# Performance work log

Measured on AMD Instinct MI355X. Metric: run time of the kernel, lower is better.

## Reference

```python
import jax, jax.numpy as jnp
import numpy as np

MASK_FILL = -1e9  # masked_fill_value (avoids NaNs vs -inf)

def setup_inputs() -> dict:
    key = jax.random.key(0)
    k1, k2, k3 = jax.random.split(key, 3)
    B, L, H, E = 4, 2048, 16, 128
    S, D = L, E
    queries = jax.random.normal(k1, (B, L, H, E), dtype=jnp.float32)
    keys = jax.random.normal(k2, (B, S, H, E), dtype=jnp.float32)
    values = jax.random.normal(k3, (B, S, H, D), dtype=jnp.float32)
    return {"queries": queries, "keys": keys, "values": values}

def reference(queries, keys, values):
    B, L, H, E = queries.shape
    S = keys.shape[1]
    scale = 1.0 / jnp.sqrt(jnp.asarray(E, queries.dtype))
    # compute_scores: dot-product scores (B,H,L,S)
    scores = jnp.einsum('blhe,bshe->bhls', queries, keys)
    # causal mask (mask_flag=True, attn_mask=None -> TriangularCausalMask)
    causal = jnp.triu(jnp.ones((L, S), dtype=bool), k=1)  # True above diagonal = masked
    scores = jnp.where(causal[None, None, :, :], MASK_FILL, scores)
    # scale * scores -> softmax (dropout p=0, eval)
    A = jax.nn.softmax(scale * scores, axis=-1)
    # combine_values: (B,H,L,S) x (B,S,H,D) -> (B,L,H,D)
    V = jnp.einsum('bhls,bshd->blhd', A, values)
    return V
```

## Files before the change

### kernel.cpp

```cpp
#include <hip/hip_runtime.h>
#include <hip/hip_bf16.h>

typedef __attribute__((ext_vector_type(4))) float f32x4;
typedef __attribute__((ext_vector_type(2))) float f32x2v;
typedef __attribute__((ext_vector_type(16))) float f32x16;
typedef __attribute__((ext_vector_type(8))) short s16x8;
typedef __attribute__((ext_vector_type(4))) short s16x4;
typedef __attribute__((ext_vector_type(4))) unsigned u32x4v;
typedef __attribute__((ext_vector_type(2))) int i32x2;

static constexpr int Bb = 4, Ll = 2048, Hh = 16, Ee = 128;
static constexpr int RS = Hh * Ee;
static constexpr float SCALE = 0.088388347648318447f;
static constexpr float LOG2E = 1.4426950408889634f;
static constexpr float SCL = SCALE * LOG2E;
static constexpr float MOFF = 26.0f;

static constexpr int KROW = 272;
static constexpr int KBYTES = 32 * KROW;
static constexpr int VROW = 80;
static constexpr int VBYTES = 128 * VROW;
static constexpr int BUFSZ = KBYTES + VBYTES;

__device__ __forceinline__ unsigned pk2bf(float lo, float hi) {
  float2 t = make_float2(lo, hi);
  __hip_bfloat162 b2 = __float22bfloat162_rn(t);
  union { __hip_bfloat162 b; unsigned u; } cv; cv.b = b2;
  return cv.u;
}

__device__ __forceinline__ s16x8 pack8(float a0, float a1, float a2, float a3,
                                       float a4, float a5, float a6, float a7) {
  u32x4v u = { pk2bf(a0,a1), pk2bf(a2,a3), pk2bf(a4,a5), pk2bf(a6,a7) };
  return *(s16x8*)&u;
}

__device__ __forceinline__ void plswap(int &x, int &y, int h5) {
#if __has_builtin(__builtin_amdgcn_permlane32_swap)
  i32x2 r = __builtin_amdgcn_permlane32_swap(x, y, false, false);
  x = r[0]; y = r[1];
#else
  int px = __shfl_xor(x, 32, 64);
  int py = __shfl_xor(y, 32, 64);
  int nx = h5 ? py : x;
  int ny = h5 ? y : px;
  x = nx; y = ny;
#endif
}

__device__ __forceinline__ s16x8 mkpa(float p0, float p1, float p2, float p3,
                                      float p4, float p5, float p6, float p7, int h5) {
  int uA = (int)pk2bf(p0, p1), uB = (int)pk2bf(p2, p3);
  int uC = (int)pk2bf(p4, p5), uD = (int)pk2bf(p6, p7);
  plswap(uA, uC, h5);
  plswap(uB, uD, h5);
  u32x4v u = { (unsigned)uA, (unsigned)uB, (unsigned)uC, (unsigned)uD };
  return *(s16x8*)&u;
}

__device__ __forceinline__ void gl_lds16(const short* g, short* l) {
  __builtin_amdgcn_global_load_lds((const __attribute__((address_space(1))) void*)g,
                                   (__attribute__((address_space(3))) void*)l, 16, 0, 0);
}

__global__ __launch_bounds__(256) void conv_k(const float* __restrict__ src, short* __restrict__ dst) {
  size_t i = ((size_t)blockIdx.x * 256 + threadIdx.x) * 8;
  f32x4 a = *(const f32x4*)(src + i);
  f32x4 b = *(const f32x4*)(src + i + 4);
  *(s16x8*)(dst + i) = pack8(a[0],a[1],a[2],a[3],b[0],b[1],b[2],b[3]);
}

__global__ __launch_bounds__(256) void conv_vt(const float* __restrict__ V, unsigned* __restrict__ Vt32) {
  const int bh = blockIdx.x >> 4, s0 = (blockIdx.x & 15) * 128;
  const int b = bh >> 4, h = bh & 15;
  const int w = threadIdx.x >> 6, lane = threadIdx.x & 63;
  const float* base = V + ((size_t)(b * Ll + s0 + 32 * w)) * RS + h * Ee + 2 * lane;
  unsigned w0[16], w1[16];
#pragma unroll
  for (int j = 0; j < 16; ++j) {
    f32x2v a = *(const f32x2v*)(base + (size_t)(2 * j) * RS);
    f32x2v c = *(const f32x2v*)(base + (size_t)(2 * j + 1) * RS);
    w0[j] = pk2bf(a[0], c[0]);
    w1[j] = pk2bf(a[1], c[1]);
  }
  unsigned* r0 = Vt32 + ((size_t)(bh * 128 + 2 * lane)) * 1024 + (s0 + 32 * w) / 2;
  unsigned* r1 = r0 + 1024;
#pragma unroll
  for (int jj = 0; jj < 4; ++jj) {
    *(u32x4v*)(r0 + 4 * jj) = (u32x4v){w0[4*jj], w0[4*jj+1], w0[4*jj+2], w0[4*jj+3]};
    *(u32x4v*)(r1 + 4 * jj) = (u32x4v){w1[4*jj], w1[4*jj+1], w1[4*jj+2], w1[4*jj+3]};
  }
}

__global__ __launch_bounds__(256, 3)
void attn_main(const float* __restrict__ Qg, const short* __restrict__ Kws,
               const short* __restrict__ Vtws, float* __restrict__ Og) {
  const int phys = blockIdx.x;
  const int qi = ((phys >> 6) & 1) ? (phys >> 7) : (15 - (phys >> 7));
  const int bh = phys & 63;
  const int b = bh >> 4, h = bh & 15;
  const int qb = qi * 128;
  const int tid = threadIdx.x, w = tid >> 6, l = tid & 63;
  const int l31 = l & 31, h5 = l >> 5;

  __shared__ __align__(16) short smem[BUFSZ];

  s16x8 qfrag[8];
  {
    const float* qp = Qg + ((size_t)(b * Ll + qb + 32 * w + l31)) * RS + h * Ee;
#pragma unroll
    for (int ks = 0; ks < 8; ++ks) {
      const int e0 = 16 * ks + 8 * h5;
      f32x4 f0 = *(const f32x4*)(qp + e0);
      f32x4 f1 = *(const f32x4*)(qp + e0 + 4);
      qfrag[ks] = pack8(f0[0]*SCL, f0[1]*SCL, f0[2]*SCL, f0[3]*SCL,
                        f1[0]*SCL, f1[1]*SCL, f1[2]*SCL, f1[3]*SCL);
    }
  }

  f32x16 acc[4];
#pragma unroll
  for (int dt = 0; dt < 4; ++dt)
#pragma unroll
    for (int r = 0; r < 16; ++r) acc[dt][r] = 0.f;
  float lacc = 0.f;

  const short* skp[3]; const short* svp[3];
  int kdst[3], vdst[3];
#pragma unroll
  for (int j = 0; j < 3; ++j) {
    const int kid = (j < 2) ? (w * 136 + 64 * j + l) : (w * 136 + 128 + (l & 7));
    const int kr = kid / 17;
    int ksl = kid % 17; if (ksl == 16) ksl = 0;
    skp[j] = Kws + ((size_t)(b * Ll + kr)) * 2048 + h * 128 + ksl * 8;
    kdst[j] = kid * 16;
    const int vid = (j < 2) ? (w * 160 + 64 * j + l) : (w * 160 + 128 + (l & 31));
    const int vr = vid / 5;
    int vsl = vid % 5; if (vsl == 4) vsl = 0;
    svp[j] = Vtws + ((size_t)(bh * 128 + vr)) * 2048 + vsl * 8;
    vdst[j] = KBYTES + vid * 16;
  }

#define STAGE(cb, kvb) do { \
    gl_lds16(skp[0] + (size_t)(kvb) * 2048, (short*)((char*)smem + (cb) + kdst[0])); \
    gl_lds16(skp[1] + (size_t)(kvb) * 2048, (short*)((char*)smem + (cb) + kdst[1])); \
    if (l < 8)  gl_lds16(skp[2] + (size_t)(kvb) * 2048, (short*)((char*)smem + (cb) + kdst[2])); \
    gl_lds16(svp[0] + (kvb), (short*)((char*)smem + (cb) + vdst[0])); \
    gl_lds16(svp[1] + (kvb), (short*)((char*)smem + (cb) + vdst[1])); \
    if (l < 32) gl_lds16(svp[2] + (kvb), (short*)((char*)smem + (cb) + vdst[2])); \
  } while (0)

  const int ntiles = 4 * qi + 4;
  const int tmaxw = 4 * qi + w;

  STAGE(0, 0);

  for (int t = 0; t < ntiles; ++t) {
    const int cbase = (t & 1) ? BUFSZ : 0;
    if (t + 1 < ntiles) {
      STAGE(cbase ? 0 : BUFSZ, 32 * (t + 1));
      asm volatile("s_waitcnt vmcnt(6)" ::: "memory");
    } else {
      asm volatile("s_waitcnt vmcnt(0)" ::: "memory");
    }
    __builtin_amdgcn_s_barrier();
    __builtin_amdgcn_sched_barrier(0);

    if (t <= tmaxw) {
      f32x16 s;
#pragma unroll
      for (int r = 0; r < 16; ++r) s[r] = 0.f;
      __builtin_amdgcn_s_setprio(1);
#pragma unroll
      for (int ks = 0; ks < 8; ++ks) {
        s16x8 a = *(const s16x8*)((const char*)smem + cbase + l31 * KROW + h5 * 16 + ks * 32);
        s = __builtin_amdgcn_mfma_f32_32x32x16_bf16(a, qfrag[ks], s, 0, 0, 0);
      }
      __builtin_amdgcn_s_setprio(0);

      if (t == tmaxw) {
#pragma unroll
        for (int r = 0; r < 16; ++r) {
          const int kvl = (r & 3) + 8 * (r >> 2) + 4 * h5;
          if (kvl > l31) s[r] = -3.0e38f;
        }
      }

      float pv[16];
#pragma unroll
      for (int r = 0; r < 16; ++r) { const float p2 = exp2f(s[r] - MOFF); pv[r] = p2; lacc += p2; }
      s16x8 pa0 = mkpa(pv[0], pv[1], pv[2], pv[3], pv[4], pv[5], pv[6], pv[7], h5);
      s16x8 pa1 = mkpa(pv[8], pv[9], pv[10], pv[11], pv[12], pv[13], pv[14], pv[15], h5);

      __builtin_amdgcn_s_setprio(1);
#pragma unroll
      for (int dt = 0; dt < 4; ++dt) {
        const int vb = cbase + KBYTES + dt * (32 * VROW) + l31 * VROW + h5 * 16;
        s16x8 av0 = *(const s16x8*)((const char*)smem + vb);
        acc[dt] = __builtin_amdgcn_mfma_f32_32x32x16_bf16(av0, pa0, acc[dt], 0, 0, 0);
        s16x8 av1 = *(const s16x8*)((const char*)smem + vb + 32);
        acc[dt] = __builtin_amdgcn_mfma_f32_32x32x16_bf16(av1, pa1, acc[dt], 0, 0, 0);
      }
      __builtin_amdgcn_s_setprio(0);
    }
    __builtin_amdgcn_sched_barrier(0);
    __builtin_amdgcn_s_barrier();
  }
#undef STAGE

  float lsum;
  {
    int pb = __builtin_bit_cast(int, lacc), pc = pb;
    plswap(pb, pc, h5);
    lsum = __builtin_bit_cast(float, pb) + __builtin_bit_cast(float, pc);
  }
  const float linv = 1.0f / lsum;

  float* orow = Og + ((size_t)(b * Ll + qb + 32 * w + l31)) * RS + h * Ee;
#pragma unroll
  for (int dt = 0; dt < 4; ++dt)
#pragma unroll
    for (int g = 0; g < 4; ++g) {
      f32x4 v = { acc[dt][4*g] * linv, acc[dt][4*g+1] * linv,
                  acc[dt][4*g+2] * linv, acc[dt][4*g+3] * linv };
      *(f32x4*)(orow + dt * 32 + g * 8 + h5 * 4) = v;
    }
}

static constexpr int VPAD = 66;
__device__ __forceinline__ short f2bf(float f) {
  union { float f; unsigned u; } x; x.f = f;
  unsigned r = x.u + 0x7FFFu + ((x.u >> 16) & 1u);
  return (short)(r >> 16);
}
__global__ __launch_bounds__(256, 4)
void attn_fwd(const float* __restrict__ Qg, const float* __restrict__ Kg,
              const float* __restrict__ Vg, float* __restrict__ Og) {
  const int qi = blockIdx.x;
  const int bh = blockIdx.y;
  const int b = bh >> 4, h = bh & 15;
  const int qb = qi * 64;
  const int tid = threadIdx.x, wave = tid >> 6, lane = tid & 63, lo = lane & 15, hi = lane >> 4;
  __shared__ __align__(16) short Klds[64 * 128];
  __shared__ __align__(16) short Vt[128 * VPAD];
  const float* Qb_ = Qg + (size_t)b * Ll * RS + h * Ee;
  const float* Kb_ = Kg + (size_t)b * Ll * RS + h * Ee;
  const float* Vb_ = Vg + (size_t)b * Ll * RS + h * Ee;
  float* Ob_ = Og + (size_t)b * Ll * RS + h * Ee;
  s16x8 qfrag[4];
  {
    const float* qp = Qb_ + (size_t)(qb + wave * 16 + lo) * RS;
#pragma unroll
    for (int ks = 0; ks < 4; ++ks) {
      const int e0 = 32 * ks + 8 * hi;
      f32x4 f0 = *(const f32x4*)(qp + e0);
      f32x4 f1 = *(const f32x4*)(qp + e0 + 4);
      qfrag[ks] = pack8(f0[0]*SCALE, f0[1]*SCALE, f0[2]*SCALE, f0[3]*SCALE,
                        f1[0]*SCALE, f1[1]*SCALE, f1[2]*SCALE, f1[3]*SCALE);
    }
  }
  f32x4 acc[8];
#pragma unroll
  for (int nt = 0; nt < 8; ++nt) acc[nt] = (f32x4){0.f, 0.f, 0.f, 0.f};
  float mrun = -3.0e38f, lrun = 0.f;
  const int r0 = tid >> 4, c0 = (tid & 15) * 8;
  for (int kvb = 0; kvb <= qb; kvb += 64) {
    __syncthreads();
#pragma unroll
    for (int rr4 = 0; rr4 < 4; ++rr4) {
      const int rr = r0 + 16 * rr4;
      const float* kp = Kb_ + (size_t)(kvb + rr) * RS + c0;
      f32x4 f0 = *(const f32x4*)kp;
      f32x4 f1 = *(const f32x4*)(kp + 4);
      const int off = (rr * 256 + c0 * 2) ^ ((rr & 7) << 4);
      *(s16x8*)((char*)Klds + off) = pack8(f0[0],f0[1],f0[2],f0[3],f1[0],f1[1],f1[2],f1[3]);
    }
#pragma unroll
    for (int kk = 0; kk < 2; ++kk) {
      const int kv0 = (r0 * 2 + kk) * 2;
      const float* vp0 = Vb_ + (size_t)(kvb + kv0) * RS + c0;
      const float* vp1 = vp0 + RS;
      f32x4 a0 = *(const f32x4*)vp0, a1 = *(const f32x4*)(vp0 + 4);
      f32x4 b0 = *(const f32x4*)vp1, b1 = *(const f32x4*)(vp1 + 4);
#pragma unroll
      for (int jj = 0; jj < 4; ++jj)
        *(unsigned*)&Vt[(c0 + jj) * VPAD + kv0] = pk2bf(a0[jj], b0[jj]);
#pragma unroll
      for (int jj = 0; jj < 4; ++jj)
        *(unsigned*)&Vt[(c0 + 4 + jj) * VPAD + kv0] = pk2bf(a1[jj], b1[jj]);
    }
    __syncthreads();
    const bool diag = (kvb == qb);
    f32x4 st[4];
#pragma unroll
    for (int mt = 0; mt < 4; ++mt) {
      f32x4 a4 = (f32x4){0.f, 0.f, 0.f, 0.f};
#pragma unroll
      for (int ks = 0; ks < 4; ++ks) {
        const int row = 16 * mt + lo;
        const int off = (row * 256 + (32 * ks + 8 * hi) * 2) ^ ((row & 7) << 4);
        s16x8 a = *(const s16x8*)((const char*)Klds + off);
        a4 = __builtin_amdgcn_mfma_f32_16x16x32_bf16(a, qfrag[ks], a4, 0, 0, 0);
      }
      st[mt] = a4;
    }
    if (diag) {
      const int qg = 16 * wave + lo;
#pragma unroll
      for (int mt = 0; mt < 4; ++mt)
#pragma unroll
        for (int r = 0; r < 4; ++r)
          if (16 * mt + 4 * hi + r > qg) st[mt][r] = -3.0e38f;
    }
    float mx = -3.0e38f;
#pragma unroll
    for (int mt = 0; mt < 4; ++mt)
#pragma unroll
      for (int r = 0; r < 4; ++r) mx = fmaxf(mx, st[mt][r]);
    mx = fmaxf(mx, __shfl_xor(mx, 16, 64));
    mx = fmaxf(mx, __shfl_xor(mx, 32, 64));
    const float mnew = fmaxf(mrun, mx);
    const float alpha = exp2f((mrun - mnew) * LOG2E);
    float psum = 0.f;
    s16x4 pf[4];
#pragma unroll
    for (int mt = 0; mt < 4; ++mt)
#pragma unroll
      for (int r = 0; r < 4; ++r) {
        const float p = exp2f((st[mt][r] - mnew) * LOG2E);
        psum += p;
        pf[mt][r] = f2bf(p);
      }
    psum += __shfl_xor(psum, 16, 64);
    psum += __shfl_xor(psum, 32, 64);
    lrun = lrun * alpha + psum;
    mrun = mnew;
    float alr[4];
#pragma unroll
    for (int r = 0; r < 4; ++r) alr[r] = __shfl(alpha, 4 * hi + r, 64);
#pragma unroll
    for (int nt = 0; nt < 8; ++nt) {
      acc[nt][0] *= alr[0]; acc[nt][1] *= alr[1];
      acc[nt][2] *= alr[2]; acc[nt][3] *= alr[3];
    }
#pragma unroll
    for (int mt = 0; mt < 4; ++mt)
#pragma unroll
      for (int nt = 0; nt < 8; ++nt) {
        const int hw = (16 * nt + lo) * VPAD + 16 * mt + 4 * hi;
        s16x4 vf = *(const s16x4*)&Vt[hw];
        acc[nt] = __builtin_amdgcn_mfma_f32_16x16x16bf16_1k(pf[mt], vf, acc[nt], 0, 0, 0);
      }
  }
  float linv[4];
#pragma unroll
  for (int r = 0; r < 4; ++r) linv[r] = 1.0f / __shfl(lrun, 4 * hi + r, 64);
#pragma unroll
  for (int r = 0; r < 4; ++r) {
    const int qg = qb + 16 * wave + 4 * hi + r;
    float* op = Ob_ + (size_t)qg * RS + lo;
#pragma unroll
    for (int nt = 0; nt < 8; ++nt)
      op[16 * nt] = acc[nt][r] * linv[r];
  }
}

extern "C" void kernel_launch(void* const* d_in, const int* in_sizes, int n_in,
                              void* d_out, int out_size, void* d_ws, size_t ws_size,
                              hipStream_t stream) {
  const float* Qp = (const float*)d_in[0];
  const float* Kp = (const float*)d_in[1];
  const float* Vp = (const float*)d_in[2];
  float* Op = (float*)d_out;
  const size_t elems = (size_t)Bb * Ll * Hh * Ee;
  if (ws_size >= elems * 2 * 2) {
    short* Kws = (short*)d_ws;
    short* Vtws = Kws + elems;
    conv_k<<<(int)(elems / 8 / 256), 256, 0, stream>>>(Kp, Kws);
    conv_vt<<<Bb * Hh * (Ll / 128), 256, 0, stream>>>(Vp, (unsigned*)Vtws);
    attn_main<<<1024, 256, 0, stream>>>(Qp, Kws, Vtws, Op);
  } else {
    dim3 grid(Ll / 64, Bb * Hh);
    attn_fwd<<<grid, 256, 0, stream>>>(Qp, Kp, Vp, Op);
  }
}
```

Baseline: 157.5 us.

## Double KV tile size to 64 rows per pipeline stage

Each pipelined KV tile grows from 32 to 64 keys, so the K/V LDS buffers are enlarged and staged with more async global-to-LDS loads. The iteration count halves, which cuts per-tile barriers and waitcnt stalls, and each wave now computes two 32-key score blocks per tile. The diagonal tile is handled per wave with a conditional second half and a new causal-mask offset. The cost is higher LDS usage, which may lower occupancy, plus more register pressure and some wasted work on partially masked tiles.

```diff
diff --git a/kernel.cpp b/kernel.cpp
--- a/kernel.cpp
+++ b/kernel.cpp
@@ -17,8 +17,8 @@
 static constexpr float MOFF = 26.0f;
 
 static constexpr int KROW = 272;
-static constexpr int KBYTES = 32 * KROW;
-static constexpr int VROW = 80;
+static constexpr int KBYTES = 64 * KROW;
+static constexpr int VROW = 144;
 static constexpr int VBYTES = 128 * VROW;
 static constexpr int BUFSZ = KBYTES + VBYTES;
 
@@ -125,18 +125,18 @@
     for (int r = 0; r < 16; ++r) acc[dt][r] = 0.f;
   float lacc = 0.f;
 
-  const short* skp[3]; const short* svp[3];
-  int kdst[3], vdst[3];
-#pragma unroll
-  for (int j = 0; j < 3; ++j) {
-    const int kid = (j < 2) ? (w * 136 + 64 * j + l) : (w * 136 + 128 + (l & 7));
+  const short* skp[5]; const short* svp[5];
+  int kdst[5], vdst[5];
+#pragma unroll
+  for (int j = 0; j < 5; ++j) {
+    const int kid = (j < 4) ? (w * 272 + 64 * j + l) : (w * 272 + 256 + (l & 15));
     const int kr = kid / 17;
     int ksl = kid % 17; if (ksl == 16) ksl = 0;
     skp[j] = Kws + ((size_t)(b * Ll + kr)) * 2048 + h * 128 + ksl * 8;
     kdst[j] = kid * 16;
-    const int vid = (j < 2) ? (w * 160 + 64 * j + l) : (w * 160 + 128 + (l & 31));
-    const int vr = vid / 5;
-    int vsl = vid % 5; if (vsl == 4) vsl = 0;
+    const int vid = (j < 4) ? (w * 288 + 64 * j + l) : (w * 288 + 256 + (l & 31));
+    const int vr = vid / 9;
+    int vsl = vid % 9; if (vsl == 8) vsl = 0;
     svp[j] = Vtws + ((size_t)(bh * 128 + vr)) * 2048 + vsl * 8;
     vdst[j] = KBYTES + vid * 16;
   }
@@ -144,22 +144,26 @@
 #define STAGE(cb, kvb) do { \
     gl_lds16(skp[0] + (size_t)(kvb) * 2048, (short*)((char*)smem + (cb) + kdst[0])); \
     gl_lds16(skp[1] + (size_t)(kvb) * 2048, (short*)((char*)smem + (cb) + kdst[1])); \
-    if (l < 8)  gl_lds16(skp[2] + (size_t)(kvb) * 2048, (short*)((char*)smem + (cb) + kdst[2])); \
+    gl_lds16(skp[2] + (size_t)(kvb) * 2048, (short*)((char*)smem + (cb) + kdst[2])); \
+    gl_lds16(skp[3] + (size_t)(kvb) * 2048, (short*)((char*)smem + (cb) + kdst[3])); \
+    if (l < 16) gl_lds16(skp[4] + (size_t)(kvb) * 2048, (short*)((char*)smem + (cb) + kdst[4])); \
     gl_lds16(svp[0] + (kvb), (short*)((char*)smem + (cb) + vdst[0])); \
     gl_lds16(svp[1] + (kvb), (short*)((char*)smem + (cb) + vdst[1])); \
-    if (l < 32) gl_lds16(svp[2] + (kvb), (short*)((char*)smem + (cb) + vdst[2])); \
+    gl_lds16(svp[2] + (kvb), (short*)((char*)smem + (cb) + vdst[2])); \
+    gl_lds16(svp[3] + (kvb), (short*)((char*)smem + (cb) + vdst[3])); \
+    if (l < 32) gl_lds16(svp[4] + (kvb), (short*)((char*)smem + (cb) + vdst[4])); \
   } while (0)
 
-  const int ntiles = 4 * qi + 4;
-  const int tmaxw = 4 * qi + w;
+  const int ntiles = 2 * qi + 2;
+  const int tmaxw = 2 * qi + (w >> 1);
 
   STAGE(0, 0);
 
   for (int t = 0; t < ntiles; ++t) {
     const int cbase = (t & 1) ? BUFSZ : 0;
     if (t + 1 < ntiles) {
-      STAGE(cbase ? 0 : BUFSZ, 32 * (t + 1));
-      asm volatile("s_waitcnt vmcnt(6)" ::: "memory");
+      STAGE(cbase ? 0 : BUFSZ, 64 * (t + 1));
+      asm volatile("s_waitcnt vmcnt(10)" ::: "memory");
     } else {
       asm volatile("s_waitcnt vmcnt(0)" ::: "memory");
     }
@@ -167,39 +171,70 @@
     __builtin_amdgcn_sched_barrier(0);
 
     if (t <= tmaxw) {
-      f32x16 s;
-#pragma unroll
-      for (int r = 0; r < 16; ++r) s[r] = 0.f;
+      const bool full2 = (t < tmaxw) || (w & 1);
+
+      f32x16 s0, s1;
+#pragma unroll
+      for (int r = 0; r < 16; ++r) { s0[r] = 0.f; s1[r] = 0.f; }
       __builtin_amdgcn_s_setprio(1);
 #pragma unroll
       for (int ks = 0; ks < 8; ++ks) {
-        s16x8 a = *(const s16x8*)((const char*)smem + cbase + l31 * KROW + h5 * 16 + ks * 32);
-        s = __builtin_amdgcn_mfma_f32_32x32x16_bf16(a, qfrag[ks], s, 0, 0, 0);
+        s16x8 a0 = *(const s16x8*)((const char*)smem + cbase + l31 * KROW + ks * 32 + h5 * 16);
+        s0 = __builtin_amdgcn_mfma_f32_32x32x16_bf16(a0, qfrag[ks], s0, 0, 0, 0);
+      }
+      if (full2) {
+#pragma unroll
+        for (int ks = 0; ks < 8; ++ks) {
+          s16x8 a1 = *(const s16x8*)((const char*)smem + cbase + (32 + l31) * KROW + ks * 32 + h5 * 16);
+          s1 = __builtin_amdgcn_mfma_f32_32x32x16_bf16(a1, qfrag[ks], s1, 0, 0, 0);
+        }
       }
       __builtin_amdgcn_s_setprio(0);
 
       if (t == tmaxw) {
+        const int qoff = qb + 32 * w - 64 * t + l31;
 #pragma unroll
         for (int r = 0; r < 16; ++r) {
-          const int kvl = (r & 3) + 8 * (r >> 2) + 4 * h5;
-          if (kvl > l31) s[r] = -3.0e38f;
+          const int kv = (r & 3) + 8 * (r >> 2) + 4 * h5;
+          if (kv > qoff) s0[r] = -3.0e38f;
         }
-      }
-
-      float pv[16];
-#pragma unroll
-      for (int r = 0; r < 16; ++r) { const float p2 = exp2f(s[r] - MOFF); pv[r] = p2; lacc += p2; }
-      s16x8 pa0 = mkpa(pv[0], pv[1], pv[2], pv[3], pv[4], pv[5], pv[6], pv[7], h5);
-      s16x8 pa1 = mkpa(pv[8], pv[9], pv[10], pv[11], pv[12], pv[13], pv[14], pv[15], h5);
+        if (full2) {
+#pragma unroll
+          for (int r = 0; r < 16; ++r) {
+            const int kv = 32 + (r & 3) + 8 * (r >> 2) + 4 * h5;
+            if (kv > qoff) s1[r] = -3.0e38f;
+          }
+        }
+      }
+
+      float pv0[16], pv1[16];
+#pragma unroll
+      for (int r = 0; r < 16; ++r) { const float p2 = exp2f(s0[r] - MOFF); pv0[r] = p2; lacc += p2; }
+      if (full2) {
+#pragma unroll
+        for (int r = 0; r < 16; ++r) { const float p2 = exp2f(s1[r] - MOFF); pv1[r] = p2; lacc += p2; }
+      }
+      s16x8 pa[4];
+      pa[0] = mkpa(pv0[0],pv0[1],pv0[2],pv0[3],pv0[4],pv0[5],pv0[6],pv0[7], h5);
+      pa[1] = mkpa(pv0[8],pv0[9],pv0[10],pv0[11],pv0[12],pv0[13],pv0[14],pv0[15], h5);
+      if (full2) {
+        pa[2] = mkpa(pv1[0],pv1[1],pv1[2],pv1[3],pv1[4],pv1[5],pv1[6],pv1[7], h5);
+        pa[3] = mkpa(pv1[8],pv1[9],pv1[10],pv1[11],pv1[12],pv1[13],pv1[14],pv1[15], h5);
+      } else {
+        pa[2] = pa[0]; pa[3] = pa[1];
+      }
 
       __builtin_amdgcn_s_setprio(1);
 #pragma unroll
       for (int dt = 0; dt < 4; ++dt) {
-        const int vb = cbase + KBYTES + dt * (32 * VROW) + l31 * VROW + h5 * 16;
-        s16x8 av0 = *(const s16x8*)((const char*)smem + vb);
-        acc[dt] = __builtin_amdgcn_mfma_f32_32x32x16_bf16(av0, pa0, acc[dt], 0, 0, 0);
-        s16x8 av1 = *(const s16x8*)((const char*)smem + vb + 32);
-        acc[dt] = __builtin_amdgcn_mfma_f32_32x32x16_bf16(av1, pa1, acc[dt], 0, 0, 0);
+        const int vb = cbase + KBYTES + (32 * dt + l31) * VROW + h5 * 16;
+#pragma unroll
+        for (int ks = 0; ks < 4; ++ks) {
+          if (ks < 2 || full2) {
+            s16x8 av = *(const s16x8*)((const char*)smem + vb + ks * 32);
+            acc[dt] = __builtin_amdgcn_mfma_f32_32x32x16_bf16(av, pa[ks], acc[dt], 0, 0, 0);
+          }
+        }
       }
       __builtin_amdgcn_s_setprio(0);
     }
```

Result: slower. 178.8 us (+13.5%).
